# Performance work log

Measured on AMD Instinct MI355X. Metric: run time of the kernel, lower is better.

Reference implementation:

```python
import jax, jax.numpy as jnp
import numpy as np

B, SRC_L, DST_L, D = 1024, 256, 256, 64

def setup_inputs() -> dict:
    key = jax.random.key(0)
    k1, k2, k3, k4, k5, k6 = jax.random.split(key, 6)
    src_ids = jax.random.randint(k1, (B, SRC_L), 0, 10000, dtype=jnp.int32)
    dst_ids = jax.random.randint(k2, (B, DST_L), 0, 10000, dtype=jnp.int32)
    s1 = 1.0  # fan_in of first Linear is 1
    s2 = 1.0 / np.sqrt(D)
    W1 = jax.random.normal(k3, (D, 1), jnp.float32) * s1
    b1 = jax.random.normal(k4, (D,), jnp.float32) * s1
    W2 = jax.random.normal(k5, (D, D), jnp.float32) * s2
    b2 = jax.random.normal(k6, (D,), jnp.float32) * s2
    return {"src_ids": src_ids, "dst_ids": dst_ids, "W1": W1, "b1": b1, "W2": W2, "b2": b2}


def _appearances(src_ids, dst_ids):
    # count(x in seq) == sum over seq of (x == seq_j); exactly matches unique+bincount lookup
    src_in_src = (src_ids[:, :, None] == src_ids[:, None, :]).sum(-1)  # [B, Ls]
    dst_in_dst = (dst_ids[:, :, None] == dst_ids[:, None, :]).sum(-1)  # [B, Ld]
    eq_sd = src_ids[:, :, None] == dst_ids[:, None, :]                 # [B, Ls, Ld]
    src_in_dst = eq_sd.sum(-1)   # [B, Ls]
    dst_in_src = eq_sd.sum(1)    # [B, Ld]
    app_src = jnp.stack([src_in_src, src_in_dst], axis=-1).astype(jnp.float32)  # [B, Ls, 2]
    app_dst = jnp.stack([dst_in_src, dst_in_dst], axis=-1).astype(jnp.float32)  # [B, Ld, 2]
    app_src = jnp.where((src_ids == 0)[:, :, None], 0.0, app_src)
    app_dst = jnp.where((dst_ids == 0)[:, :, None], 0.0, app_dst)
    return app_src, app_dst


def _mlp_sum(app, W1, b1, W2, b2):
    # Linear(1,D) -> ReLU -> Linear(D,D), then sum over the 2 co-occurrence channels
    h = jax.nn.relu(app[..., None] * W1[:, 0] + b1)      # [B, L, 2, D]
    out = jnp.einsum('blcd,ed->blce', h, W2) + b2         # [B, L, 2, D]
    return out.sum(axis=2)                                # [B, L, D]


def reference(src_ids, dst_ids, W1, b1, W2, b2):
    app_src, app_dst = _appearances(src_ids, dst_ids)
    src_feat = _mlp_sum(app_src, W1, b1, W2, b2)
    dst_feat = _mlp_sum(app_dst, W1, b1, W2, b2)
    return (src_feat, dst_feat)
```

## Files before the change

### kernel.cpp

```cpp
#include <hip/hip_runtime.h>

#define BATCH 1024
#define L 256
#define D 64
#define NIDS 10000
#define TABN 257

typedef float f32x4 __attribute__((ext_vector_type(4)));

__global__ __launch_bounds__(256) void build_table_kernel(
        const float* __restrict__ W1,
        const float* __restrict__ b1,
        const float* __restrict__ W2,
        const float* __restrict__ b2,
        float* __restrict__ tab) {
    const int t = blockIdx.x * 256 + threadIdx.x;
    const int a = t >> 6;
    const int e = t & 63;
    if (a >= TABN) return;
    const float af = (float)a;
    float acc = b2[e];
    #pragma unroll
    for (int d = 0; d < D; ++d) {
        float h = fmaf(af, W1[d], b1[d]);
        h = fmaxf(h, 0.0f);
        acc = fmaf(h, W2[e * D + d], acc);
    }
    tab[a * D + e] = acc;
}

__global__ __launch_bounds__(256) void cooc_kernel(
        const int* __restrict__ src_ids,
        const int* __restrict__ dst_ids,
        const float* __restrict__ tab,
        float* __restrict__ out) {
    __shared__ alignas(16) unsigned int hist[NIDS / 2];
    __shared__ unsigned int cnts[2 * L];

    const int b   = blockIdx.x;
    const int tid = threadIdx.x;

    const int sid = src_ids[b * L + tid];
    const int did = dst_ids[b * L + tid];

    uint4* h4 = (uint4*)hist;

    for (int i = tid; i < NIDS / 8; i += 256) h4[i] = make_uint4(0u, 0u, 0u, 0u);
    __syncthreads();
    atomicAdd(&hist[sid >> 1], 1u << ((sid & 1) * 16));
    __syncthreads();
    unsigned c_ss = (hist[sid >> 1] >> ((sid & 1) * 16)) & 0xffffu;
    unsigned c_ds = (hist[did >> 1] >> ((did & 1) * 16)) & 0xffffu;
    __syncthreads();

    for (int i = tid; i < NIDS / 8; i += 256) h4[i] = make_uint4(0u, 0u, 0u, 0u);
    __syncthreads();
    atomicAdd(&hist[did >> 1], 1u << ((did & 1) * 16));
    __syncthreads();
    unsigned c_sd = (hist[sid >> 1] >> ((sid & 1) * 16)) & 0xffffu;
    unsigned c_dd = (hist[did >> 1] >> ((did & 1) * 16)) & 0xffffu;

    if (sid == 0) { c_ss = 0u; c_sd = 0u; }
    if (did == 0) { c_ds = 0u; c_dd = 0u; }
    cnts[tid]     = c_ss | (c_sd << 16);
    cnts[L + tid] = c_ds | (c_dd << 16);
    __syncthreads();

    const f32x4* tab4 = (const f32x4*)tab;
    f32x4*       out4 = (f32x4*)out;
    const int q    = tid & 15;
    const int pg   = tid >> 4;
    const int ROW4 = D / 4;

    f32x4* osrc = out4 + (size_t)b * (L * ROW4);
    f32x4* odst = out4 + (size_t)BATCH * L * ROW4 + (size_t)b * (L * ROW4);

    #pragma unroll 4
    for (int p = pg; p < L; p += 16) {
        const unsigned cp = cnts[p];
        const f32x4 v1 = tab4[(cp & 0xffffu) * ROW4 + q];
        const f32x4 v2 = tab4[(cp >> 16) * ROW4 + q];
        __builtin_nontemporal_store(v1 + v2, &osrc[p * ROW4 + q]);
    }
    #pragma unroll 4
    for (int p = pg; p < L; p += 16) {
        const unsigned cp = cnts[L + p];
        const f32x4 v1 = tab4[(cp & 0xffffu) * ROW4 + q];
        const f32x4 v2 = tab4[(cp >> 16) * ROW4 + q];
        __builtin_nontemporal_store(v1 + v2, &odst[p * ROW4 + q]);
    }
}

extern "C" void kernel_launch(void* const* d_in, const int* in_sizes, int n_in,
                              void* d_out, int out_size, void* d_ws, size_t ws_size,
                              hipStream_t stream) {
    const int*   src_ids = (const int*)d_in[0];
    const int*   dst_ids = (const int*)d_in[1];
    const float* W1      = (const float*)d_in[2];
    const float* b1      = (const float*)d_in[3];
    const float* W2      = (const float*)d_in[4];
    const float* b2      = (const float*)d_in[5];
    float*       out     = (float*)d_out;
    float*       tab     = (float*)d_ws;

    build_table_kernel<<<(TABN * 64 + 255) / 256, 256, 0, stream>>>(W1, b1, W2, b2, tab);
    cooc_kernel<<<BATCH, 256, 0, stream>>>(src_ids, dst_ids, tab, out);
}
```

Baseline: 153.8 us.

## Split co-occurrence kernel into src/dst halves with cumulative histogram

```diff
diff --git a/kernel.cpp b/kernel.cpp
--- a/kernel.cpp
+++ b/kernel.cpp
@@ -29,65 +29,56 @@
     tab[a * D + e] = acc;
 }
 
-__global__ __launch_bounds__(256) void cooc_kernel(
+__global__ __launch_bounds__(256, 8) void cooc_kernel(
         const int* __restrict__ src_ids,
         const int* __restrict__ dst_ids,
         const float* __restrict__ tab,
         float* __restrict__ out) {
     __shared__ alignas(16) unsigned int hist[NIDS / 2];
-    __shared__ unsigned int cnts[2 * L];
 
-    const int b   = blockIdx.x;
-    const int tid = threadIdx.x;
+    const int bid  = blockIdx.x;
+    const int b    = bid >> 1;
+    const int half = bid & 1;
+    const int tid  = threadIdx.x;
 
-    const int sid = src_ids[b * L + tid];
-    const int did = dst_ids[b * L + tid];
+    const int sid  = src_ids[b * L + tid];
+    const int did  = dst_ids[b * L + tid];
+    const int myid = half ? did : sid;
 
     uint4* h4 = (uint4*)hist;
-
+    #pragma unroll
     for (int i = tid; i < NIDS / 8; i += 256) h4[i] = make_uint4(0u, 0u, 0u, 0u);
     __syncthreads();
+
     atomicAdd(&hist[sid >> 1], 1u << ((sid & 1) * 16));
     __syncthreads();
-    unsigned c_ss = (hist[sid >> 1] >> ((sid & 1) * 16)) & 0xffffu;
-    unsigned c_ds = (hist[did >> 1] >> ((did & 1) * 16)) & 0xffffu;
+    const unsigned r1 = (hist[myid >> 1] >> ((myid & 1) * 16)) & 0xffffu;
     __syncthreads();
 
-    for (int i = tid; i < NIDS / 8; i += 256) h4[i] = make_uint4(0u, 0u, 0u, 0u);
-    __syncthreads();
     atomicAdd(&hist[did >> 1], 1u << ((did & 1) * 16));
     __syncthreads();
-    unsigned c_sd = (hist[sid >> 1] >> ((sid & 1) * 16)) & 0xffffu;
-    unsigned c_dd = (hist[did >> 1] >> ((did & 1) * 16)) & 0xffffu;
+    const unsigned r2 = (hist[myid >> 1] >> ((myid & 1) * 16)) & 0xffffu;
 
-    if (sid == 0) { c_ss = 0u; c_sd = 0u; }
-    if (did == 0) { c_ds = 0u; c_dd = 0u; }
-    cnts[tid]     = c_ss | (c_sd << 16);
-    cnts[L + tid] = c_ds | (c_dd << 16);
+    unsigned c1 = r1;
+    unsigned c2 = r2 - r1;
+    if (myid == 0) { c1 = 0u; c2 = 0u; }
+    __syncthreads();
+
+    hist[tid] = c1 | (c2 << 16);
     __syncthreads();
 
     const f32x4* tab4 = (const f32x4*)tab;
-    f32x4*       out4 = (f32x4*)out;
-    const int q    = tid & 15;
-    const int pg   = tid >> 4;
-    const int ROW4 = D / 4;
-
-    f32x4* osrc = out4 + (size_t)b * (L * ROW4);
-    f32x4* odst = out4 + (size_t)BATCH * L * ROW4 + (size_t)b * (L * ROW4);
+    f32x4* o = (f32x4*)out + (size_t)(half * BATCH + b) * (L * 16);
+    const int q  = tid & 15;
+    const int pg = tid >> 4;
 
     #pragma unroll 4
-    for (int p = pg; p < L; p += 16) {
-        const unsigned cp = cnts[p];
-        const f32x4 v1 = tab4[(cp & 0xffffu) * ROW4 + q];
-        const f32x4 v2 = tab4[(cp >> 16) * ROW4 + q];
-        __builtin_nontemporal_store(v1 + v2, &osrc[p * ROW4 + q]);
-    }
-    #pragma unroll 4
-    for (int p = pg; p < L; p += 16) {
-        const unsigned cp = cnts[L + p];
-        const f32x4 v1 = tab4[(cp & 0xffffu) * ROW4 + q];
-        const f32x4 v2 = tab4[(cp >> 16) * ROW4 + q];
-        __builtin_nontemporal_store(v1 + v2, &odst[p * ROW4 + q]);
+    for (int k = 0; k < 16; ++k) {
+        const int p = pg + 16 * k;
+        const unsigned cp = hist[p];
+        const f32x4 v1 = tab4[(cp & 0xffffu) * 16 + q];
+        const f32x4 v2 = tab4[(cp >> 16) * 16 + q];
+        __builtin_nontemporal_store(v1 + v2, &o[p * 16 + q]);
     }
 }
 
@@ -104,5 +95,5 @@
     float*       tab     = (float*)d_ws;
 
     build_table_kernel<<<(TABN * 64 + 255) / 256, 256, 0, stream>>>(W1, b1, W2, b2, tab);
-    cooc_kernel<<<BATCH, 256, 0, stream>>>(src_ids, dst_ids, tab, out);
+    cooc_kernel<<<2 * BATCH, 256, 0, stream>>>(src_ids, dst_ids, tab, out);
 }
```

New measurement: 153.4 us. About the same (-0.3%).
